# Kernel tuning notes

Measured on AMD Instinct MI355X. Metric: run time of the kernel, lower is better.

## Reference

```python
import jax, jax.numpy as jnp
from jax import lax
import numpy as np

B = 4096

def _conv(x, w, b):
    # x: [B,C,H,W], w: [O,I,3,3] torch OIHW layout, VALID, stride 1
    y = lax.conv_general_dilated(x, w, (1, 1), 'VALID',
                                 dimension_numbers=('NCHW', 'OIHW', 'NCHW'))
    return y + b[None, :, None, None]

def _pool2(x):
    return lax.reduce_window(x, -jnp.inf, lax.max, (1, 1, 2, 2), (1, 1, 2, 2), 'VALID')

def _lin(x, w, b):
    # torch Linear: y = x @ W^T + b, W: [out, in]
    return x @ w.T + b

def setup_inputs() -> dict:
    key = jax.random.key(0)
    ks = jax.random.split(key, 24)
    def w(k, shape, fan_in):
        return (jax.random.normal(k, shape, dtype=jnp.float32) / np.sqrt(fan_in)).astype(jnp.float32)
    inp = {
        'x':      jax.random.normal(ks[0], (B, 1, 28, 28), dtype=jnp.float32),
        'c1_w':   w(ks[1], (50, 1, 3, 3), 9),      'c1_b':  jnp.zeros((50,), jnp.float32),
        'c2_w':   w(ks[2], (50, 50, 3, 3), 450),   'c2_b':  jnp.zeros((50,), jnp.float32),
        'c3_w':   w(ks[3], (50, 50, 3, 3), 450),   'c3_b':  jnp.zeros((50,), jnp.float32),
        'l1c1_w': w(ks[4], (500, 50 * 13 * 13), 50 * 13 * 13), 'l1c1_b': jnp.zeros((500,), jnp.float32),
        'l2c1_w': w(ks[5], (10, 500), 500),        'l2c1_b': jnp.zeros((10,), jnp.float32),
        'l1c2_w': w(ks[6], (500, 50 * 5 * 5), 50 * 5 * 5),     'l1c2_b': jnp.zeros((500,), jnp.float32),
        'l2c2_w': w(ks[7], (10, 500), 500),        'l2c2_b': jnp.zeros((10,), jnp.float32),
        'l1_w':   w(ks[8], (500, 50), 50),         'l1_b':  jnp.zeros((500,), jnp.float32),
        'l2_w':   w(ks[9], (10, 500), 500),        'l2_b':  jnp.zeros((10,), jnp.float32),
        'd1_w':   w(ks[10], (2, 50 * 13 * 13), 50 * 13 * 13),  'd1_b':  jnp.zeros((2,), jnp.float32),
        'd2_w':   w(ks[11], (2, 50 * 5 * 5), 50 * 5 * 5),      'd2_b':  jnp.zeros((2,), jnp.float32),
    }
    return inp

def reference(x, c1_w, c1_b, c2_w, c2_b, c3_w, c3_b,
              l1c1_w, l1c1_b, l2c1_w, l2c1_b,
              l1c2_w, l1c2_b, l2c2_w, l2c2_b,
              l1_w, l1_b, l2_w, l2_b, d1_w, d1_b, d2_w, d2_b):
    b = x.shape[0]
    # stage 1
    h1 = _pool2(jax.nn.relu(_conv(x, c1_w, c1_b)))           # [B,50,13,13]
    f1 = h1.reshape(b, 50 * 13 * 13)
    exit1 = jnp.argmax(_lin(f1, d1_w, d1_b), axis=1) == 0     # [B] bool
    out1 = _lin(_lin(f1, l1c1_w, l1c1_b), l2c1_w, l2c1_b)     # [B,10] (no relu, as in source)
    # stage 2 (computed densely; selection below replicates the gather/scatter routing)
    h2 = _pool2(jax.nn.relu(_conv(h1, c2_w, c2_b)))          # [B,50,5,5]
    f2 = h2.reshape(b, 50 * 5 * 5)
    exit2 = jnp.argmax(_lin(f2, d2_w, d2_b), axis=1) == 0
    out2 = _lin(_lin(f2, l1c2_w, l1c2_b), l2c2_w, l2c2_b)
    # stage 3
    h3 = _pool2(jax.nn.relu(_conv(h2, c3_w, c3_b)))          # [B,50,1,1]
    f3 = h3.reshape(b, 50)
    out3 = _lin(jax.nn.relu(_lin(f3, l1_w, l1_b)), l2_w, l2_b)
    sel = jnp.where(exit1[:, None], out1, jnp.where(exit2[:, None], out2, out3))
    # original returns cat(out1_subset, out2_subset, out3_subset) + an index order;
    # we return the equivalent per-sample outputs in original batch order.
    return jax.nn.log_softmax(sel, axis=1)
```

## Files before the change

### kernel.cpp

```cpp
#include <hip/hip_runtime.h>
#include <hip/hip_bf16.h>
#include <cstdint>


typedef __bf16 bf16_t;
typedef __bf16 bf16x8 __attribute__((ext_vector_type(8)));
typedef float  f32x4  __attribute__((ext_vector_type(4)));

#define B_IMG 4096


__device__ void role_conv1(char* smem, int blk,
    const float* __restrict__ x, const float* __restrict__ w1,
    const float* __restrict__ b1, float* __restrict__ h1)
{
    float* ws = (float*)smem;
    float* bs = ws + 456;
    const int t = threadIdx.x;
    for (int i = t; i < 450; i += 256) ws[i] = w1[i];
    if (t < 50) bs[t] = b1[t];
    __syncthreads();

    const int idx = blk * 256 + t;
    if (idx >= B_IMG * 169) return;
    const int b   = idx / 169;
    const int pos = idx % 169;
    const int py = pos / 13, px = pos % 13;

    const float* xp = x + (size_t)b * 784 + (2 * py) * 28 + 2 * px;
    float p[4][4];
#pragma unroll
    for (int r = 0; r < 4; ++r)
#pragma unroll
        for (int c = 0; c < 4; ++c) p[r][c] = xp[r * 28 + c];

    float* hb = h1 + (size_t)b * 8480 + pos;
    if (pos < 30) h1[(size_t)b * 8480 + 8450 + pos] = 0.f;

    for (int oc = 0; oc < 50; ++oc) {
        const float* wp = &ws[oc * 9];
        const float w00 = wp[0], w01 = wp[1], w02 = wp[2];
        const float w10 = wp[3], w11 = wp[4], w12 = wp[5];
        const float w20 = wp[6], w21 = wp[7], w22 = wp[8];
        float a[2][2];
#pragma unroll
        for (int dy = 0; dy < 2; ++dy)
#pragma unroll
            for (int dx = 0; dx < 2; ++dx) {
                a[dy][dx] = p[dy + 0][dx + 0] * w00 + p[dy + 0][dx + 1] * w01 + p[dy + 0][dx + 2] * w02
                          + p[dy + 1][dx + 0] * w10 + p[dy + 1][dx + 1] * w11 + p[dy + 1][dx + 2] * w12
                          + p[dy + 2][dx + 0] * w20 + p[dy + 2][dx + 1] * w21 + p[dy + 2][dx + 2] * w22;
            }
        float v = fmaxf(fmaxf(a[0][0], a[0][1]), fmaxf(a[1][0], a[1][1])) + bs[oc];
        hb[oc * 169] = fmaxf(v, 0.f);
    }
}

__device__ void role_wb16(int blk, const float* __restrict__ src,
                          bf16_t* __restrict__ dst, int N, int K, int Kp, int total)
{
    const int idx = blk * 256 + threadIdx.x;
    if (idx >= total) return;
    const int n = idx / Kp, k = idx % Kp;
    const float v = (n < N && k < K) ? src[(size_t)n * K + k] : 0.f;
    dst[idx] = (bf16_t)v;
}

__device__ void role_w2t(int blk, const float* __restrict__ w2, float* __restrict__ w2p)
{
    const int idx = blk * 256 + threadIdx.x;
    if (idx >= 50 * 600) return;
    const int ic = idx / 600, r = idx % 600, oc = r / 12, j = r % 12;
    w2p[idx] = (j < 9) ? w2[oc * 450 + ic * 9 + j] : 0.f;
}

__device__ void role_conv2(char* smem, int b,
    const float* __restrict__ h1, const float* __restrict__ w2p,
    const float* __restrict__ b2, float* __restrict__ h2)
{
    float* in   = (float*)smem;
    float* wbuf = in + 1360;
    const int t = threadIdx.x;

    for (int s = t; s < 676; s += 256) in[s] = h1[(size_t)b * 8480 + s];
    {
        const float4* src = (const float4*)w2p;
        float4* dst = (float4*)wbuf;
        for (int s = t; s < 600; s += 256) dst[s] = src[s];
    }
    __syncthreads();
    if (t < 30) h2[(size_t)b * 1280 + 1250 + t] = 0.f;

    const int ocg = t / 25;
    const int pos = t % 25;
    const int py = pos / 5, px = pos % 5;
    const int oc0 = ocg * 5;
    const bool act = (t < 250);

    float acc[5][4];
#pragma unroll
    for (int j = 0; j < 5; ++j)
#pragma unroll
        for (int q = 0; q < 4; ++q) acc[j][q] = 0.f;

    for (int ic0 = 0; ic0 < 50; ic0 += 4) {
        const int cur = (ic0 >> 2) & 1;
        if (ic0 + 4 < 50) {
            const int nxt = cur ^ 1;
            const int nic2 = (50 - ic0 - 4 < 4) ? (50 - ic0 - 4) : 4;
            for (int s = t; s < nic2 * 169; s += 256)
                in[nxt * 680 + s] = h1[(size_t)b * 8480 + (ic0 + 4) * 169 + s];
            const float4* src = (const float4*)(w2p + (size_t)(ic0 + 4) * 600);
            float4* dst = (float4*)(wbuf + nxt * 2400);
            for (int s = t; s < nic2 * 150; s += 256) dst[s] = src[s];
        }
        if (act) {
            const int nic = (50 - ic0 < 4) ? (50 - ic0) : 4;
            const float* ibc = in + cur * 680 + (2 * py) * 13 + 2 * px;
            for (int icl = 0; icl < nic; ++icl) {
                float p[4][4];
                const float* ip = ibc + icl * 169;
#pragma unroll
                for (int r = 0; r < 4; ++r)
#pragma unroll
                    for (int c = 0; c < 4; ++c) p[r][c] = ip[r * 13 + c];
                const float* wl = wbuf + cur * 2400 + icl * 600 + oc0 * 12;
#pragma unroll
                for (int j = 0; j < 5; ++j) {
                    const f32x4 wv0 = *(const f32x4*)(wl + j * 12);
                    const f32x4 wv1 = *(const f32x4*)(wl + j * 12 + 4);
                    const f32x4 wv2 = *(const f32x4*)(wl + j * 12 + 8);
                    const float w00 = wv0[0], w01 = wv0[1], w02 = wv0[2];
                    const float w10 = wv0[3], w11 = wv1[0], w12 = wv1[1];
                    const float w20 = wv1[2], w21 = wv1[3], w22 = wv2[0];
#pragma unroll
                    for (int dy = 0; dy < 2; ++dy)
#pragma unroll
                        for (int dx = 0; dx < 2; ++dx) {
                            acc[j][dy * 2 + dx] +=
                                  p[dy + 0][dx + 0] * w00 + p[dy + 0][dx + 1] * w01 + p[dy + 0][dx + 2] * w02
                                + p[dy + 1][dx + 0] * w10 + p[dy + 1][dx + 1] * w11 + p[dy + 1][dx + 2] * w12
                                + p[dy + 2][dx + 0] * w20 + p[dy + 2][dx + 1] * w21 + p[dy + 2][dx + 2] * w22;
                        }
                }
            }
        }
        __syncthreads();
    }

    if (act) {
#pragma unroll
        for (int j = 0; j < 5; ++j) {
            float v = fmaxf(fmaxf(acc[j][0], acc[j][1]), fmaxf(acc[j][2], acc[j][3]));
            h2[(size_t)b * 1280 + (oc0 + j) * 25 + pos] = fmaxf(v + b2[oc0 + j], 0.f);
        }
    }
}

__device__ void role_conv3(char* smem, int blk,
    const float* __restrict__ h2, const float* __restrict__ w3,
    const float* __restrict__ b3, float* __restrict__ f3)
{
    float* in = (float*)smem;
    const int t = threadIdx.x;
    for (int i = t; i < 5000; i += 256) {
        const int img = i / 1250, off = i % 1250;
        in[i] = h2[(size_t)(blk * 4 + img) * 1280 + off];
    }
    __syncthreads();
    const int il = t >> 6;
    const int oc = t & 63;
    if (oc >= 50) return;

    const float* ip0 = &in[il * 1250];
    float a00 = 0.f, a01 = 0.f, a10 = 0.f, a11 = 0.f;
    for (int ic = 0; ic < 50; ++ic) {
        float p[4][4];
        const float* ip = ip0 + ic * 25;
#pragma unroll
        for (int r = 0; r < 4; ++r)
#pragma unroll
            for (int c = 0; c < 4; ++c) p[r][c] = ip[r * 5 + c];
        const float* wp = &w3[((size_t)oc * 50 + ic) * 9];
        const float w00 = wp[0], w01 = wp[1], w02 = wp[2];
        const float w10 = wp[3], w11 = wp[4], w12 = wp[5];
        const float w20 = wp[6], w21 = wp[7], w22 = wp[8];
        a00 += p[0][0]*w00 + p[0][1]*w01 + p[0][2]*w02 + p[1][0]*w10 + p[1][1]*w11 + p[1][2]*w12 + p[2][0]*w20 + p[2][1]*w21 + p[2][2]*w22;
        a01 += p[0][1]*w00 + p[0][2]*w01 + p[0][3]*w02 + p[1][1]*w10 + p[1][2]*w11 + p[1][3]*w12 + p[2][1]*w20 + p[2][2]*w21 + p[2][3]*w22;
        a10 += p[1][0]*w00 + p[1][1]*w01 + p[1][2]*w02 + p[2][0]*w10 + p[2][1]*w11 + p[2][2]*w12 + p[3][0]*w20 + p[3][1]*w21 + p[3][2]*w22;
        a11 += p[1][1]*w00 + p[1][2]*w01 + p[1][3]*w02 + p[2][1]*w10 + p[2][2]*w11 + p[2][3]*w12 + p[3][1]*w20 + p[3][2]*w21 + p[3][3]*w22;
    }
    float v = fmaxf(fmaxf(a00, a01), fmaxf(a10, a11)) + b3[oc];
    f3[(size_t)(blk * 4 + il) * 50 + oc] = fmaxf(v, 0.f);
}

__device__ void role_exit(char* smem, int b,
    const float* __restrict__ F, int ldf, int K,
    const float* __restrict__ dw, const float* __restrict__ db, int* __restrict__ e)
{
    float* r0 = (float*)smem;
    float* r1 = r0 + 256;
    const int t = threadIdx.x;
    const float* f = F + (size_t)b * ldf;
    float s0 = 0.f, s1 = 0.f;
    for (int i = t; i < K; i += 256) {
        const float v = f[i];
        s0 += v * dw[i];
        s1 += v * dw[K + i];
    }
    r0[t] = s0; r1[t] = s1;
    __syncthreads();
    for (int s = 128; s > 0; s >>= 1) {
        if (t < s) { r0[t] += r0[t + s]; r1[t] += r1[t + s]; }
        __syncthreads();
    }
    if (t == 0) e[b] = (r0[0] + db[0] >= r1[0] + db[1]) ? 1 : 0;
}

__device__ void role_gemm(char* smem, int g,
    const float* __restrict__ A, int lda, const bf16_t* __restrict__ W,
    const float* __restrict__ bias, float* __restrict__ C0, float* __restrict__ C1,
    int Kp, int khalf, int Nout, int ldc)
{
    bf16_t* As = (bf16_t*)smem;
    bf16_t* Bs = As + 128 * 40;

    const int t = threadIdx.x;
    const int m0 = (g & 31) * 128;
    const int n0 = ((g >> 5) & 7) * 64;
    const int kz = g >> 8;
    const int kbeg = kz ? khalf : 0;
    const int kend = kz ? Kp : khalf;
    float* C = kz ? C1 : C0;

    const int wave = t >> 6;
    const int lane = t & 63;
    const int wm = (wave >> 1) * 64;
    const int wn = (wave & 1) * 32;
    const int quad = lane >> 4;
    const int lr = lane & 15;

    f32x4 acc[4][2];
#pragma unroll
    for (int i = 0; i < 4; ++i)
#pragma unroll
        for (int j = 0; j < 2; ++j) acc[i][j] = (f32x4)0.f;

    const int ar = t >> 2;
    const int ac = (t & 3) * 8;

    for (int k0 = kbeg; k0 < kend; k0 += 32) {
        __syncthreads();
#pragma unroll
        for (int h = 0; h < 2; ++h) {
            const float* ap = A + (size_t)(m0 + ar + h * 64) * lda + k0 + ac;
            const float4 f0 = *(const float4*)ap;
            const float4 f1 = *(const float4*)(ap + 4);
            bf16x8 v;
            v[0] = (bf16_t)f0.x; v[1] = (bf16_t)f0.y; v[2] = (bf16_t)f0.z; v[3] = (bf16_t)f0.w;
            v[4] = (bf16_t)f1.x; v[5] = (bf16_t)f1.y; v[6] = (bf16_t)f1.z; v[7] = (bf16_t)f1.w;
            *(bf16x8*)&As[(ar + h * 64) * 40 + ac] = v;
        }
        *(uint4*)&Bs[ar * 40 + ac] = *(const uint4*)&W[(size_t)(n0 + ar) * Kp + k0 + ac];
        __syncthreads();

        bf16x8 af[4], bfr[2];
#pragma unroll
        for (int i = 0; i < 4; ++i)
            af[i] = *(const bf16x8*)&As[(wm + i * 16 + lr) * 40 + quad * 8];
#pragma unroll
        for (int j = 0; j < 2; ++j)
            bfr[j] = *(const bf16x8*)&Bs[(wn + j * 16 + lr) * 40 + quad * 8];
#pragma unroll
        for (int i = 0; i < 4; ++i)
#pragma unroll
            for (int j = 0; j < 2; ++j)
                acc[i][j] = __builtin_amdgcn_mfma_f32_16x16x32_bf16(af[i], bfr[j], acc[i][j], 0, 0, 0);
    }

#pragma unroll
    for (int j = 0; j < 2; ++j) {
        const int n = n0 + wn + j * 16 + lr;
        const float bv = (kz == 0 && n < Nout) ? bias[n] : 0.f;
#pragma unroll
        for (int i = 0; i < 4; ++i) {
            const int mrow = m0 + wm + i * 16 + quad * 4;
#pragma unroll
            for (int r = 0; r < 4; ++r)
                C[(size_t)(mrow + r) * ldc + n] = acc[i][j][r] + bv;
        }
    }
}

__device__ void role_lin10(char* smem, int blk,
    const float* __restrict__ U, const float* __restrict__ U2, int ldu,
    const float* __restrict__ W, const float* __restrict__ bias,
    float* __restrict__ out)
{
    float* red = (float*)smem;
    const int t = threadIdx.x;
    const int ks = t & 15;
    const int il = t >> 4;
    const int b  = blk * 16 + il;
    const float* u = U + (size_t)b * ldu;

    float acc[10];
#pragma unroll
    for (int o = 0; o < 10; ++o) acc[o] = 0.f;

    if (U2) {
        const float* u2 = U2 + (size_t)b * ldu;
        for (int i = 0; i < 31; ++i) {
            const int k = ks + i * 16;
            const float uv = u[k] + u2[k];
#pragma unroll
            for (int o = 0; o < 10; ++o) acc[o] += uv * W[o * 500 + k];
        }
        const int k = ks + 496;
        if (k < 500) {
            const float uv = u[k] + u2[k];
#pragma unroll
            for (int o = 0; o < 10; ++o) acc[o] += uv * W[o * 500 + k];
        }
    } else {
        for (int i = 0; i < 31; ++i) {
            const int k = ks + i * 16;
            const float uv = u[k];
#pragma unroll
            for (int o = 0; o < 10; ++o) acc[o] += uv * W[o * 500 + k];
        }
        const int k = ks + 496;
        if (k < 500) {
            const float uv = u[k];
#pragma unroll
            for (int o = 0; o < 10; ++o) acc[o] += uv * W[o * 500 + k];
        }
    }
#pragma unroll
    for (int o = 0; o < 10; ++o) red[(il * 10 + o) * 17 + ks] = acc[o];
    __syncthreads();
    if (t < 160) {
        const int il2 = t / 10, o = t - il2 * 10;
        float s = 0.f;
#pragma unroll
        for (int q = 0; q < 16; ++q) s += red[(il2 * 10 + o) * 17 + q];
        out[(size_t)(blk * 16 + il2) * 10 + o] = s + bias[o];
    }
}


__global__ __launch_bounds__(256) void k_prep(
    const float* x, const float* c1w, const float* c1b, float* h1,
    const float* l1c1w, bf16_t* Wb1, const float* l1c2w, bf16_t* Wb2,
    const float* c2w, float* w2p)
{
    extern __shared__ char smem[];
    const int g = blockIdx.x;
    if (g < 2704)        role_conv1(smem, g, x, c1w, c1b, h1);
    else if (g < 19664)  role_wb16(g - 2704, l1c1w, Wb1, 500, 8450, 8480, 512 * 8480);
    else if (g < 22224)  role_wb16(g - 19664, l1c2w, Wb2, 500, 1250, 1280, 512 * 1280);
    else                 role_w2t(g - 22224, c2w, w2p);
}

__global__ __launch_bounds__(256) void k_stage1(
    const float* h1, const bf16_t* Wb1, const float* l1c1b, float* u, float* up,
    const float* d1w, const float* d1b, int* e1,
    const float* w2p, const float* c2b, float* h2)
{
    extern __shared__ char smem[];
    const int g = blockIdx.x;
    if (g < 512)         role_gemm(smem, g, h1, 8480, Wb1, l1c1b, u, up, 8480, 4256, 500, 512);
    else if (g < 4608)   role_conv2(smem, g - 512, h1, w2p, c2b, h2);
    else                 role_exit(smem, g - 4608, h1, 8480, 8450, d1w, d1b, e1);
}

__global__ __launch_bounds__(256) void k_stage2(
    const float* h2, const bf16_t* Wb2, const float* l1c2b, float* v, float* vp,
    const float* d2w, const float* d2b, int* e2,
    const float* c3w, const float* c3b, float* f3,
    const float* u, const float* up, const float* l2c1w, const float* l2c1b, float* out1)
{
    extern __shared__ char smem[];
    const int g = blockIdx.x;
    if (g < 512)         role_gemm(smem, g, h2, 1280, Wb2, l1c2b, v, vp, 1280, 640, 500, 512);
    else if (g < 1536)   role_conv3(smem, g - 512, h2, c3w, c3b, f3);
    else if (g < 1792)   role_lin10(smem, g - 1536, u, up, 512, l2c1w, l2c1b, out1);
    else                 role_exit(smem, g - 1792, h2, 1280, 1250, d2w, d2b, e2);
}

__global__ __launch_bounds__(256) void k_tail(
    const float* __restrict__ v, const float* __restrict__ vp,
    const float* __restrict__ l2c2w, const float* __restrict__ l2c2b,
    const float* __restrict__ f3, const float* __restrict__ l1w, const float* __restrict__ l1b,
    const float* __restrict__ l2w, const float* __restrict__ l2b,
    const float* __restrict__ out1, const int* __restrict__ e1, const int* __restrict__ e2,
    float* __restrict__ out)
{
    __shared__ float fs[800];
    __shared__ float u3loc[8000];
    __shared__ float red[2720];
    __shared__ float o2loc[160];
    __shared__ float o3loc[160];

    const int t   = threadIdx.x;
    const int blk = blockIdx.x;
    const int ks  = t & 15;
    const int il  = t >> 4;

    for (int i = t; i < 800; i += 256) fs[i] = f3[(size_t)blk * 800 + i];
    __syncthreads();

    for (int im = 0; im < 16; ++im) {
        for (int o = t; o < 500; o += 256) {
            float s = 0.f;
#pragma unroll
            for (int k = 0; k < 50; ++k) s += fs[im * 50 + k] * l1w[o * 50 + k];
            u3loc[im * 500 + o] = fmaxf(s + l1b[o], 0.f);
        }
    }

    {
        const float* uu  = v  + (size_t)(blk * 16 + il) * 512;
        const float* uu2 = vp + (size_t)(blk * 16 + il) * 512;
        float acc[10];
#pragma unroll
        for (int o = 0; o < 10; ++o) acc[o] = 0.f;
        for (int i = 0; i < 31; ++i) {
            const int k = ks + i * 16;
            const float uv = uu[k] + uu2[k];
#pragma unroll
            for (int o = 0; o < 10; ++o) acc[o] += uv * l2c2w[o * 500 + k];
        }
        const int k = ks + 496;
        if (k < 500) {
            const float uv = uu[k] + uu2[k];
#pragma unroll
            for (int o = 0; o < 10; ++o) acc[o] += uv * l2c2w[o * 500 + k];
        }
        __syncthreads();
#pragma unroll
        for (int o = 0; o < 10; ++o) red[(il * 10 + o) * 17 + ks] = acc[o];
        __syncthreads();
        if (t < 160) {
            const int il2 = t / 10, o = t - il2 * 10;
            float s = 0.f;
#pragma unroll
            for (int q = 0; q < 16; ++q) s += red[(il2 * 10 + o) * 17 + q];
            o2loc[t] = s + l2c2b[o];
        }
        __syncthreads();
    }

    {
        const float* uu = u3loc + il * 500;
        float acc[10];
#pragma unroll
        for (int o = 0; o < 10; ++o) acc[o] = 0.f;
        for (int i = 0; i < 31; ++i) {
            const int k = ks + i * 16;
            const float uv = uu[k];
#pragma unroll
            for (int o = 0; o < 10; ++o) acc[o] += uv * l2w[o * 500 + k];
        }
        const int k = ks + 496;
        if (k < 500) {
            const float uv = uu[k];
#pragma unroll
            for (int o = 0; o < 10; ++o) acc[o] += uv * l2w[o * 500 + k];
        }
#pragma unroll
        for (int o = 0; o < 10; ++o) red[(il * 10 + o) * 17 + ks] = acc[o];
        __syncthreads();
        if (t < 160) {
            const int il2 = t / 10, o = t - il2 * 10;
            float s = 0.f;
#pragma unroll
            for (int q = 0; q < 16; ++q) s += red[(il2 * 10 + o) * 17 + q];
            o3loc[t] = s + l2b[o];
        }
        __syncthreads();
    }

    if (t < 16) {
        const int b = blk * 16 + t;
        float vv[10];
        if (e1[b]) {
            const float* src = out1 + (size_t)b * 10;
#pragma unroll
            for (int o = 0; o < 10; ++o) vv[o] = src[o];
        } else if (e2[b]) {
#pragma unroll
            for (int o = 0; o < 10; ++o) vv[o] = o2loc[t * 10 + o];
        } else {
#pragma unroll
            for (int o = 0; o < 10; ++o) vv[o] = o3loc[t * 10 + o];
        }
        float m = -3.4e38f;
#pragma unroll
        for (int o = 0; o < 10; ++o) m = fmaxf(m, vv[o]);
        float s = 0.f;
#pragma unroll
        for (int o = 0; o < 10; ++o) s += expf(vv[o] - m);
        const float ls = logf(s);
#pragma unroll
        for (int o = 0; o < 10; ++o) out[(size_t)b * 10 + o] = vv[o] - m - ls;
    }
}

static inline size_t align256(size_t v) { return (v + 255) & ~(size_t)255; }

extern "C" void kernel_launch(void* const* d_in, const int* in_sizes, int n_in,
                              void* d_out, int out_size, void* d_ws, size_t ws_size,
                              hipStream_t stream)
{
    const float* x     = (const float*)d_in[0];
    const float* c1w   = (const float*)d_in[1];
    const float* c1b   = (const float*)d_in[2];
    const float* c2w   = (const float*)d_in[3];
    const float* c2b   = (const float*)d_in[4];
    const float* c3w   = (const float*)d_in[5];
    const float* c3b   = (const float*)d_in[6];
    const float* l1c1w = (const float*)d_in[7];
    const float* l1c1b = (const float*)d_in[8];
    const float* l2c1w = (const float*)d_in[9];
    const float* l2c1b = (const float*)d_in[10];
    const float* l1c2w = (const float*)d_in[11];
    const float* l1c2b = (const float*)d_in[12];
    const float* l2c2w = (const float*)d_in[13];
    const float* l2c2b = (const float*)d_in[14];
    const float* l1w   = (const float*)d_in[15];
    const float* l1b   = (const float*)d_in[16];
    const float* l2w   = (const float*)d_in[17];
    const float* l2b   = (const float*)d_in[18];
    const float* d1w   = (const float*)d_in[19];
    const float* d1b   = (const float*)d_in[20];
    const float* d2w   = (const float*)d_in[21];
    const float* d2b   = (const float*)d_in[22];

    size_t off = 0;
    const size_t oWb1  = off; off = align256(off + (size_t)512 * 8480 * 2);
    const size_t oWb2  = off; off = align256(off + (size_t)512 * 1280 * 2);
    const size_t oW2P  = off; off = align256(off + (size_t)50 * 600 * 4);
    const size_t oOut1 = off; off = align256(off + (size_t)B_IMG * 10 * 4);
    const size_t oE1   = off; off = align256(off + (size_t)B_IMG * 4);
    const size_t oE2   = off; off = align256(off + (size_t)B_IMG * 4);
    const size_t oH1   = off; off = align256(off + (size_t)B_IMG * 8480 * 4);
    const size_t oH2   = off; off = align256(off + (size_t)B_IMG * 1280 * 4);
    const size_t oU    = off; off = align256(off + (size_t)B_IMG * 512 * 4);
    const size_t oUP   = off; off = align256(off + (size_t)B_IMG * 512 * 4);
    const size_t oF3   = off; off = align256(off + (size_t)B_IMG * 50 * 4);

    char* ws = (char*)d_ws;
    bf16_t* Wb1  = (bf16_t*)(ws + oWb1);
    bf16_t* Wb2  = (bf16_t*)(ws + oWb2);
    float*  w2p  = (float*) (ws + oW2P);
    float*  out1 = (float*) (ws + oOut1);
    int*    e1   = (int*)   (ws + oE1);
    int*    e2   = (int*)   (ws + oE2);
    float*  h1   = (float*) (ws + oH1);
    float*  h2   = (float*) (ws + oH2);
    float*  u    = (float*) (ws + oU);
    float*  up   = (float*) (ws + oUP);
    float*  f3   = (float*) (ws + oF3);
    float*  v    = h1;
    float*  vp   = h1 + (size_t)B_IMG * 512;

    float* out = (float*)d_out;

    k_prep<<<22342, 256, 2048, stream>>>(x, c1w, c1b, h1, l1c1w, Wb1, l1c2w, Wb2, c2w, w2p);
    k_stage1<<<8704, 256, 24832, stream>>>(h1, Wb1, l1c1b, u, up, d1w, d1b, e1, w2p, c2b, h2);
    k_stage2<<<5888, 256, 20000, stream>>>(h2, Wb2, l1c2b, v, vp, d2w, d2b, e2,
                                           c3w, c3b, f3, u, up, l2c1w, l2c1b, out1);
    k_tail<<<256, 256, 0, stream>>>(v, vp, l2c2w, l2c2b, f3, l1w, l1b, l2w, l2b,
                                    out1, e1, e2, out);

    (void)in_sizes; (void)n_in; (void)out_size; (void)ws_size;
}
```

Before: 738.5 us.

## Restructure conv2 to process two images per block with register-staged prefetch

Each conv2 block now handles two images, and each thread accumulates 10 output channels instead of 5, which halves the number of conv2 blocks and doubles per-thread reuse of the loaded input patch. Weights are no longer copied to shared memory. They are read directly from global memory (expected to hit in cache), and the input is staged in chunks of 5 channels through registers and double-buffered in shared memory. The stage-1 kernel's shared-memory request is reduced and it gets a 4-blocks-per-CU occupancy hint. The trade-offs are more register pressure from 40 accumulators plus staging registers, and weight loads that now go through the cache path instead of LDS.

```diff
diff --git a/kernel.cpp b/kernel.cpp
--- a/kernel.cpp
+++ b/kernel.cpp
@@ -74,59 +74,73 @@
     w2p[idx] = (j < 9) ? w2[oc * 450 + ic * 9 + j] : 0.f;
 }
 
-__device__ void role_conv2(char* smem, int b,
+__device__ void role_conv2(char* smem, int blkpair,
     const float* __restrict__ h1, const float* __restrict__ w2p,
     const float* __restrict__ b2, float* __restrict__ h2)
 {
-    float* in   = (float*)smem;
-    float* wbuf = in + 1360;
-    const int t = threadIdx.x;
-
-    for (int s = t; s < 676; s += 256) in[s] = h1[(size_t)b * 8480 + s];
-    {
-        const float4* src = (const float4*)w2p;
-        float4* dst = (float4*)wbuf;
-        for (int s = t; s < 600; s += 256) dst[s] = src[s];
+    float* in = (float*)smem;
+    const int t  = threadIdx.x;
+    const int b0 = blkpair * 2;
+
+    for (int s = t; s < 1690; s += 256) {
+        const int img = (s >= 845);
+        const int off = s - img * 845;
+        in[s] = h1[(size_t)(b0 + img) * 8480 + off];
     }
     __syncthreads();
-    if (t < 30) h2[(size_t)b * 1280 + 1250 + t] = 0.f;
-
-    const int ocg = t / 25;
-    const int pos = t % 25;
-    const int py = pos / 5, px = pos % 5;
-    const int oc0 = ocg * 5;
+    if (t < 60) {
+        const int img = t / 30, o = t - img * 30;
+        h2[(size_t)(b0 + img) * 1280 + 1250 + o] = 0.f;
+    }
+
+    const int il  = t / 125;
+    const int tl  = t - il * 125;
+    const int ocg = tl / 25;
+    const int pos = tl - ocg * 25;
+    const int py = pos / 5, px = pos - py * 5;
+    const int oc0 = ocg * 10;
     const bool act = (t < 250);
 
-    float acc[5][4];
-#pragma unroll
-    for (int j = 0; j < 5; ++j)
+    float acc[10][4];
+#pragma unroll
+    for (int j = 0; j < 10; ++j)
 #pragma unroll
         for (int q = 0; q < 4; ++q) acc[j][q] = 0.f;
 
-    for (int ic0 = 0; ic0 < 50; ic0 += 4) {
-        const int cur = (ic0 >> 2) & 1;
-        if (ic0 + 4 < 50) {
-            const int nxt = cur ^ 1;
-            const int nic2 = (50 - ic0 - 4 < 4) ? (50 - ic0 - 4) : 4;
-            for (int s = t; s < nic2 * 169; s += 256)
-                in[nxt * 680 + s] = h1[(size_t)b * 8480 + (ic0 + 4) * 169 + s];
-            const float4* src = (const float4*)(w2p + (size_t)(ic0 + 4) * 600);
-            float4* dst = (float4*)(wbuf + nxt * 2400);
-            for (int s = t; s < nic2 * 150; s += 256) dst[s] = src[s];
-        }
+    const float* ib0 = in + il * 845 + (2 * py) * 13 + 2 * px;
+    const float* wb0 = w2p + oc0 * 12;
+
+    for (int c = 0; c < 10; ++c) {
+        const int cur = c & 1;
+
+        float stg[7];
+        if (c + 1 < 10) {
+            const int base = (c + 1) * 845;
+#pragma unroll
+            for (int u = 0; u < 7; ++u) {
+                const int s = t + u * 256;
+                if (s < 1690) {
+                    const int img = (s >= 845);
+                    const int off = s - img * 845;
+                    stg[u] = h1[(size_t)(b0 + img) * 8480 + base + off];
+                }
+            }
+        }
+
         if (act) {
-            const int nic = (50 - ic0 < 4) ? (50 - ic0) : 4;
-            const float* ibc = in + cur * 680 + (2 * py) * 13 + 2 * px;
-            for (int icl = 0; icl < nic; ++icl) {
+            const float* ibc = ib0 + cur * 1690;
+            const int ic0 = c * 5;
+#pragma unroll 1
+            for (int icl = 0; icl < 5; ++icl) {
                 float p[4][4];
                 const float* ip = ibc + icl * 169;
 #pragma unroll
                 for (int r = 0; r < 4; ++r)
 #pragma unroll
-                    for (int c = 0; c < 4; ++c) p[r][c] = ip[r * 13 + c];
-                const float* wl = wbuf + cur * 2400 + icl * 600 + oc0 * 12;
-#pragma unroll
-                for (int j = 0; j < 5; ++j) {
+                    for (int cc = 0; cc < 4; ++cc) p[r][cc] = ip[r * 13 + cc];
+                const float* wl = wb0 + (size_t)(ic0 + icl) * 600;
+#pragma unroll
+                for (int j = 0; j < 10; ++j) {
                     const f32x4 wv0 = *(const f32x4*)(wl + j * 12);
                     const f32x4 wv1 = *(const f32x4*)(wl + j * 12 + 4);
                     const f32x4 wv2 = *(const f32x4*)(wl + j * 12 + 8);
@@ -145,14 +159,23 @@
                 }
             }
         }
+
+        if (c + 1 < 10) {
+            const int nxt = cur ^ 1;
+#pragma unroll
+            for (int u = 0; u < 7; ++u) {
+                const int s = t + u * 256;
+                if (s < 1690) in[nxt * 1690 + s] = stg[u];
+            }
+        }
         __syncthreads();
     }
 
     if (act) {
 #pragma unroll
-        for (int j = 0; j < 5; ++j) {
+        for (int j = 0; j < 10; ++j) {
             float v = fmaxf(fmaxf(acc[j][0], acc[j][1]), fmaxf(acc[j][2], acc[j][3]));
-            h2[(size_t)b * 1280 + (oc0 + j) * 25 + pos] = fmaxf(v + b2[oc0 + j], 0.f);
+            h2[(size_t)(b0 + il) * 1280 + (oc0 + j) * 25 + pos] = fmaxf(v + b2[oc0 + j], 0.f);
         }
     }
 }
@@ -362,7 +385,7 @@
     else                 role_w2t(g - 22224, c2w, w2p);
 }
 
-__global__ __launch_bounds__(256) void k_stage1(
+__global__ __launch_bounds__(256, 4) void k_stage1(
     const float* h1, const bf16_t* Wb1, const float* l1c1b, float* u, float* up,
     const float* d1w, const float* d1b, int* e1,
     const float* w2p, const float* c2b, float* h2)
@@ -370,8 +393,8 @@
     extern __shared__ char smem[];
     const int g = blockIdx.x;
     if (g < 512)         role_gemm(smem, g, h1, 8480, Wb1, l1c1b, u, up, 8480, 4256, 500, 512);
-    else if (g < 4608)   role_conv2(smem, g - 512, h1, w2p, c2b, h2);
-    else                 role_exit(smem, g - 4608, h1, 8480, 8450, d1w, d1b, e1);
+    else if (g < 2560)   role_conv2(smem, g - 512, h1, w2p, c2b, h2);
+    else                 role_exit(smem, g - 2560, h1, 8480, 8450, d1w, d1b, e1);
 }
 
 __global__ __launch_bounds__(256) void k_stage2(
@@ -568,7 +591,7 @@
     float* out = (float*)d_out;
 
     k_prep<<<22342, 256, 2048, stream>>>(x, c1w, c1b, h1, l1c1w, Wb1, l1c2w, Wb2, c2w, w2p);
-    k_stage1<<<8704, 256, 24832, stream>>>(h1, Wb1, l1c1b, u, up, d1w, d1b, e1, w2p, c2b, h2);
+    k_stage1<<<6656, 256, 15488, stream>>>(h1, Wb1, l1c1b, u, up, d1w, d1b, e1, w2p, c2b, h2);
     k_stage2<<<5888, 256, 20000, stream>>>(h2, Wb2, l1c2b, v, vp, d2w, d2b, e2,
                                            c3w, c3b, f3, u, up, l2c1w, l2c1b, out1);
     k_tail<<<256, 256, 0, stream>>>(v, vp, l2c2w, l2c2b, f3, l1w, l1b, l2w, l2b,
```

Result: slower. 982.5 us (+33.0%).

## Fuse exit-classifier dot products into conv2 and conv3 blocks

Applied to the files above, without the earlier changes.

Removes the separate exit-decision blocks by computing the exit-1 dot product inside the conv2 role, using the h1 tiles it already stages in shared memory, and the exit-2 dot product inside conv3 from its staged h2. The conv2 loop is reworked to process 5 input channels per chunk, prefetching the next chunk into registers before writing it to the other shared buffer. This drops 4096+4096 blocks and the re-reads of h1/h2 from global memory. In exchange it uses more shared memory per conv2 block and adds reduction work and register pressure to the conv blocks.

```diff
diff --git a/kernel.cpp b/kernel.cpp
--- a/kernel.cpp
+++ b/kernel.cpp
@@ -76,17 +76,20 @@
 
 __device__ void role_conv2(char* smem, int b,
     const float* __restrict__ h1, const float* __restrict__ w2p,
-    const float* __restrict__ b2, float* __restrict__ h2)
+    const float* __restrict__ b2, float* __restrict__ h2,
+    const float* __restrict__ d1w, const float* __restrict__ d1b,
+    int* __restrict__ e1)
 {
     float* in   = (float*)smem;
-    float* wbuf = in + 1360;
+    float* wbuf = in + 1696;
     const int t = threadIdx.x;
-
-    for (int s = t; s < 676; s += 256) in[s] = h1[(size_t)b * 8480 + s];
+    const float* hb = h1 + (size_t)b * 8480;
+
+    for (int s = t; s < 845; s += 256) in[s] = hb[s];
     {
         const float4* src = (const float4*)w2p;
         float4* dst = (float4*)wbuf;
-        for (int s = t; s < 600; s += 256) dst[s] = src[s];
+        for (int s = t; s < 750; s += 256) dst[s] = src[s];
     }
     __syncthreads();
     if (t < 30) h2[(size_t)b * 1280 + 1250 + t] = 0.f;
@@ -103,28 +106,42 @@
 #pragma unroll
         for (int q = 0; q < 4; ++q) acc[j][q] = 0.f;
 
-    for (int ic0 = 0; ic0 < 50; ic0 += 4) {
-        const int cur = (ic0 >> 2) & 1;
-        if (ic0 + 4 < 50) {
-            const int nxt = cur ^ 1;
-            const int nic2 = (50 - ic0 - 4 < 4) ? (50 - ic0 - 4) : 4;
-            for (int s = t; s < nic2 * 169; s += 256)
-                in[nxt * 680 + s] = h1[(size_t)b * 8480 + (ic0 + 4) * 169 + s];
-            const float4* src = (const float4*)(w2p + (size_t)(ic0 + 4) * 600);
-            float4* dst = (float4*)(wbuf + nxt * 2400);
-            for (int s = t; s < nic2 * 150; s += 256) dst[s] = src[s];
-        }
+    float ex0 = 0.f, ex1 = 0.f;
+
+    const float* ib0 = in + (2 * py) * 13 + 2 * px;
+
+    for (int c = 0; c < 10; ++c) {
+        const int cur = c & 1;
+
+        float istg[4];
+        float4 wstg[3];
+        if (c < 9) {
+            const float* isrc = hb + (c + 1) * 845;
+#pragma unroll
+            for (int u = 0; u < 4; ++u) {
+                const int s = t + u * 256;
+                if (s < 845) istg[u] = isrc[s];
+            }
+            const float4* wsrc = (const float4*)(w2p + (size_t)(c + 1) * 3000);
+#pragma unroll
+            for (int u = 0; u < 3; ++u) {
+                const int s = t + u * 256;
+                if (s < 750) wstg[u] = wsrc[s];
+            }
+        }
+
         if (act) {
-            const int nic = (50 - ic0 < 4) ? (50 - ic0) : 4;
-            const float* ibc = in + cur * 680 + (2 * py) * 13 + 2 * px;
-            for (int icl = 0; icl < nic; ++icl) {
+            const float* ibc = ib0 + cur * 845;
+            const float* wcb = wbuf + cur * 3000 + oc0 * 12;
+#pragma unroll 1
+            for (int icl = 0; icl < 5; ++icl) {
                 float p[4][4];
                 const float* ip = ibc + icl * 169;
 #pragma unroll
                 for (int r = 0; r < 4; ++r)
 #pragma unroll
-                    for (int c = 0; c < 4; ++c) p[r][c] = ip[r * 13 + c];
-                const float* wl = wbuf + cur * 2400 + icl * 600 + oc0 * 12;
+                    for (int cc = 0; cc < 4; ++cc) p[r][cc] = ip[r * 13 + cc];
+                const float* wl = wcb + icl * 600;
 #pragma unroll
                 for (int j = 0; j < 5; ++j) {
                     const f32x4 wv0 = *(const f32x4*)(wl + j * 12);
@@ -145,6 +162,36 @@
                 }
             }
         }
+
+        {
+            const float* dwa = d1w + c * 845;
+            const float* dwb = d1w + 8450 + c * 845;
+            const float* inc = in + cur * 845;
+#pragma unroll
+            for (int u = 0; u < 4; ++u) {
+                const int s = t + u * 256;
+                if (s < 845) {
+                    const float vv = inc[s];
+                    ex0 += vv * dwa[s];
+                    ex1 += vv * dwb[s];
+                }
+            }
+        }
+
+        if (c < 9) {
+            const int nxt = cur ^ 1;
+#pragma unroll
+            for (int u = 0; u < 4; ++u) {
+                const int s = t + u * 256;
+                if (s < 845) in[nxt * 845 + s] = istg[u];
+            }
+            float4* wdst = (float4*)(wbuf + nxt * 3000);
+#pragma unroll
+            for (int u = 0; u < 3; ++u) {
+                const int s = t + u * 256;
+                if (s < 750) wdst[s] = wstg[u];
+            }
+        }
         __syncthreads();
     }
 
@@ -155,11 +202,28 @@
             h2[(size_t)b * 1280 + (oc0 + j) * 25 + pos] = fmaxf(v + b2[oc0 + j], 0.f);
         }
     }
-}
-
-__device__ void role_conv3(char* smem, int blk,
+
+#pragma unroll
+    for (int off = 32; off > 0; off >>= 1) {
+        ex0 += __shfl_down(ex0, off);
+        ex1 += __shfl_down(ex1, off);
+    }
+    float* r = (float*)smem;
+    const int wv = t >> 6;
+    if ((t & 63) == 0) { r[wv] = ex0; r[8 + wv] = ex1; }
+    __syncthreads();
+    if (t == 0) {
+        const float s0 = r[0] + r[1] + r[2] + r[3] + d1b[0];
+        const float s1 = r[8] + r[9] + r[10] + r[11] + d1b[1];
+        e1[b] = (s0 >= s1) ? 1 : 0;
+    }
+}
+
+__device__ void role_conv3x(char* smem, int blk,
     const float* __restrict__ h2, const float* __restrict__ w3,
-    const float* __restrict__ b3, float* __restrict__ f3)
+    const float* __restrict__ b3,
+    const float* __restrict__ d2w, const float* __restrict__ d2b,
+    int* __restrict__ e2, float* __restrict__ f3)
 {
     float* in = (float*)smem;
     const int t = threadIdx.x;
@@ -168,8 +232,26 @@
         in[i] = h2[(size_t)(blk * 4 + img) * 1280 + off];
     }
     __syncthreads();
-    const int il = t >> 6;
-    const int oc = t & 63;
+    const int il   = t >> 6;
+    const int lane = t & 63;
+
+    {
+        const float* ip = &in[il * 1250];
+        float s0 = 0.f, s1 = 0.f;
+        for (int i = lane; i < 1250; i += 64) {
+            const float vv = ip[i];
+            s0 += vv * d2w[i];
+            s1 += vv * d2w[1250 + i];
+        }
+#pragma unroll
+        for (int off = 32; off > 0; off >>= 1) {
+            s0 += __shfl_down(s0, off);
+            s1 += __shfl_down(s1, off);
+        }
+        if (lane == 0) e2[blk * 4 + il] = (s0 + d2b[0] >= s1 + d2b[1]) ? 1 : 0;
+    }
+
+    const int oc = lane;
     if (oc >= 50) return;
 
     const float* ip0 = &in[il * 1250];
@@ -194,29 +276,6 @@
     f3[(size_t)(blk * 4 + il) * 50 + oc] = fmaxf(v, 0.f);
 }
 
-__device__ void role_exit(char* smem, int b,
-    const float* __restrict__ F, int ldf, int K,
-    const float* __restrict__ dw, const float* __restrict__ db, int* __restrict__ e)
-{
-    float* r0 = (float*)smem;
-    float* r1 = r0 + 256;
-    const int t = threadIdx.x;
-    const float* f = F + (size_t)b * ldf;
-    float s0 = 0.f, s1 = 0.f;
-    for (int i = t; i < K; i += 256) {
-        const float v = f[i];
-        s0 += v * dw[i];
-        s1 += v * dw[K + i];
-    }
-    r0[t] = s0; r1[t] = s1;
-    __syncthreads();
-    for (int s = 128; s > 0; s >>= 1) {
-        if (t < s) { r0[t] += r0[t + s]; r1[t] += r1[t + s]; }
-        __syncthreads();
-    }
-    if (t == 0) e[b] = (r0[0] + db[0] >= r1[0] + db[1]) ? 1 : 0;
-}
-
 __device__ void role_gemm(char* smem, int g,
     const float* __restrict__ A, int lda, const bf16_t* __restrict__ W,
     const float* __restrict__ bias, float* __restrict__ C0, float* __restrict__ C1,
@@ -370,8 +429,7 @@
     extern __shared__ char smem[];
     const int g = blockIdx.x;
     if (g < 512)         role_gemm(smem, g, h1, 8480, Wb1, l1c1b, u, up, 8480, 4256, 500, 512);
-    else if (g < 4608)   role_conv2(smem, g - 512, h1, w2p, c2b, h2);
-    else                 role_exit(smem, g - 4608, h1, 8480, 8450, d1w, d1b, e1);
+    else                 role_conv2(smem, g - 512, h1, w2p, c2b, h2, d1w, d1b, e1);
 }
 
 __global__ __launch_bounds__(256) void k_stage2(
@@ -383,9 +441,8 @@
     extern __shared__ char smem[];
     const int g = blockIdx.x;
     if (g < 512)         role_gemm(smem, g, h2, 1280, Wb2, l1c2b, v, vp, 1280, 640, 500, 512);
-    else if (g < 1536)   role_conv3(smem, g - 512, h2, c3w, c3b, f3);
-    else if (g < 1792)   role_lin10(smem, g - 1536, u, up, 512, l2c1w, l2c1b, out1);
-    else                 role_exit(smem, g - 1792, h2, 1280, 1250, d2w, d2b, e2);
+    else if (g < 1536)   role_conv3x(smem, g - 512, h2, c3w, c3b, d2w, d2b, e2, f3);
+    else                 role_lin10(smem, g - 1536, u, up, 512, l2c1w, l2c1b, out1);
 }
 
 __global__ __launch_bounds__(256) void k_tail(
@@ -568,8 +625,8 @@
     float* out = (float*)d_out;
 
     k_prep<<<22342, 256, 2048, stream>>>(x, c1w, c1b, h1, l1c1w, Wb1, l1c2w, Wb2, c2w, w2p);
-    k_stage1<<<8704, 256, 24832, stream>>>(h1, Wb1, l1c1b, u, up, d1w, d1b, e1, w2p, c2b, h2);
-    k_stage2<<<5888, 256, 20000, stream>>>(h2, Wb2, l1c2b, v, vp, d2w, d2b, e2,
+    k_stage1<<<4608, 256, 30784, stream>>>(h1, Wb1, l1c1b, u, up, d1w, d1b, e1, w2p, c2b, h2);
+    k_stage2<<<1792, 256, 20000, stream>>>(h2, Wb2, l1c2b, v, vp, d2w, d2b, e2,
                                            c3w, c3b, f3, u, up, l2c1w, l2c1b, out1);
     k_tail<<<256, 256, 0, stream>>>(v, vp, l2c2w, l2c2b, f3, l1w, l1b, l2w, l2b,
                                     out1, e1, e2, out);
```

Result: slower. 817.0 us (+10.6%).

## Emit bf16 activation copies for GEMMs, vectorize weight conversion, fuse exit2 into conv3

Applied to the files above, without the earlier changes.

The conv1 and conv2 producers now also write bf16 copies of their activations, so the FC GEMMs load bf16 tiles directly instead of reading fp32 and converting inside the inner loop. The weight fp32-to-bf16 prep now handles eight elements per thread with a vector store, which cuts the prep grid size. The stage-2 exit classifier is folded into the conv3 blocks using wave shuffles, since those blocks already hold the h2 tile in shared memory, and its separate blocks are removed. In exchange the producers write extra bf16 buffers, adding global write traffic and workspace.

```diff
diff --git a/kernel.cpp b/kernel.cpp
--- a/kernel.cpp
+++ b/kernel.cpp
@@ -12,7 +12,8 @@
 
 __device__ void role_conv1(char* smem, int blk,
     const float* __restrict__ x, const float* __restrict__ w1,
-    const float* __restrict__ b1, float* __restrict__ h1)
+    const float* __restrict__ b1, float* __restrict__ h1,
+    bf16_t* __restrict__ h1b)
 {
     float* ws = (float*)smem;
     float* bs = ws + 456;
@@ -34,8 +35,12 @@
 #pragma unroll
         for (int c = 0; c < 4; ++c) p[r][c] = xp[r * 28 + c];
 
-    float* hb = h1 + (size_t)b * 8480 + pos;
-    if (pos < 30) h1[(size_t)b * 8480 + 8450 + pos] = 0.f;
+    float*  hb  = h1  + (size_t)b * 8480 + pos;
+    bf16_t* hbb = h1b + (size_t)b * 8480 + pos;
+    if (pos < 30) {
+        h1 [(size_t)b * 8480 + 8450 + pos] = 0.f;
+        h1b[(size_t)b * 8480 + 8450 + pos] = (bf16_t)0.f;
+    }
 
     for (int oc = 0; oc < 50; ++oc) {
         const float* wp = &ws[oc * 9];
@@ -52,18 +57,28 @@
                           + p[dy + 2][dx + 0] * w20 + p[dy + 2][dx + 1] * w21 + p[dy + 2][dx + 2] * w22;
             }
         float v = fmaxf(fmaxf(a[0][0], a[0][1]), fmaxf(a[1][0], a[1][1])) + bs[oc];
-        hb[oc * 169] = fmaxf(v, 0.f);
-    }
-}
-
-__device__ void role_wb16(int blk, const float* __restrict__ src,
-                          bf16_t* __restrict__ dst, int N, int K, int Kp, int total)
+        const float r = fmaxf(v, 0.f);
+        hb [oc * 169] = r;
+        hbb[oc * 169] = (bf16_t)r;
+    }
+}
+
+__device__ void role_wb16v8(int blk, const float* __restrict__ src,
+                            bf16_t* __restrict__ dst, int N, int K, int Kp, int totalv)
 {
     const int idx = blk * 256 + threadIdx.x;
-    if (idx >= total) return;
-    const int n = idx / Kp, k = idx % Kp;
-    const float v = (n < N && k < K) ? src[(size_t)n * K + k] : 0.f;
-    dst[idx] = (bf16_t)v;
+    if (idx >= totalv) return;
+    const int kg = Kp >> 3;
+    const int n  = idx / kg;
+    const int k0 = (idx - n * kg) * 8;
+    bf16x8 v;
+#pragma unroll
+    for (int i = 0; i < 8; ++i) {
+        const int k = k0 + i;
+        const float f = (n < N && k < K) ? src[(size_t)n * K + k] : 0.f;
+        v[i] = (bf16_t)f;
+    }
+    *(bf16x8*)&dst[(size_t)n * Kp + k0] = v;
 }
 
 __device__ void role_w2t(int blk, const float* __restrict__ w2, float* __restrict__ w2p)
@@ -76,7 +91,8 @@
 
 __device__ void role_conv2(char* smem, int b,
     const float* __restrict__ h1, const float* __restrict__ w2p,
-    const float* __restrict__ b2, float* __restrict__ h2)
+    const float* __restrict__ b2, float* __restrict__ h2,
+    bf16_t* __restrict__ h2b)
 {
     float* in   = (float*)smem;
     float* wbuf = in + 1360;
@@ -89,7 +105,10 @@
         for (int s = t; s < 600; s += 256) dst[s] = src[s];
     }
     __syncthreads();
-    if (t < 30) h2[(size_t)b * 1280 + 1250 + t] = 0.f;
+    if (t < 30) {
+        h2 [(size_t)b * 1280 + 1250 + t] = 0.f;
+        h2b[(size_t)b * 1280 + 1250 + t] = (bf16_t)0.f;
+    }
 
     const int ocg = t / 25;
     const int pos = t % 25;
@@ -152,14 +171,18 @@
 #pragma unroll
         for (int j = 0; j < 5; ++j) {
             float v = fmaxf(fmaxf(acc[j][0], acc[j][1]), fmaxf(acc[j][2], acc[j][3]));
-            h2[(size_t)b * 1280 + (oc0 + j) * 25 + pos] = fmaxf(v + b2[oc0 + j], 0.f);
-        }
-    }
-}
-
-__device__ void role_conv3(char* smem, int blk,
+            const float r = fmaxf(v + b2[oc0 + j], 0.f);
+            h2 [(size_t)b * 1280 + (oc0 + j) * 25 + pos] = r;
+            h2b[(size_t)b * 1280 + (oc0 + j) * 25 + pos] = (bf16_t)r;
+        }
+    }
+}
+
+__device__ void role_conv3x(char* smem, int blk,
     const float* __restrict__ h2, const float* __restrict__ w3,
-    const float* __restrict__ b3, float* __restrict__ f3)
+    const float* __restrict__ b3,
+    const float* __restrict__ d2w, const float* __restrict__ d2b,
+    int* __restrict__ e2, float* __restrict__ f3)
 {
     float* in = (float*)smem;
     const int t = threadIdx.x;
@@ -168,8 +191,26 @@
         in[i] = h2[(size_t)(blk * 4 + img) * 1280 + off];
     }
     __syncthreads();
-    const int il = t >> 6;
-    const int oc = t & 63;
+    const int il   = t >> 6;
+    const int lane = t & 63;
+
+    {
+        const float* ip = &in[il * 1250];
+        float s0 = 0.f, s1 = 0.f;
+        for (int i = lane; i < 1250; i += 64) {
+            const float vv = ip[i];
+            s0 += vv * d2w[i];
+            s1 += vv * d2w[1250 + i];
+        }
+#pragma unroll
+        for (int off = 32; off > 0; off >>= 1) {
+            s0 += __shfl_down(s0, off);
+            s1 += __shfl_down(s1, off);
+        }
+        if (lane == 0) e2[blk * 4 + il] = (s0 + d2b[0] >= s1 + d2b[1]) ? 1 : 0;
+    }
+
+    const int oc = lane;
     if (oc >= 50) return;
 
     const float* ip0 = &in[il * 1250];
@@ -218,7 +259,7 @@
 }
 
 __device__ void role_gemm(char* smem, int g,
-    const float* __restrict__ A, int lda, const bf16_t* __restrict__ W,
+    const bf16_t* __restrict__ A, int lda, const bf16_t* __restrict__ W,
     const float* __restrict__ bias, float* __restrict__ C0, float* __restrict__ C1,
     int Kp, int khalf, int Nout, int ldc)
 {
@@ -253,13 +294,8 @@
         __syncthreads();
 #pragma unroll
         for (int h = 0; h < 2; ++h) {
-            const float* ap = A + (size_t)(m0 + ar + h * 64) * lda + k0 + ac;
-            const float4 f0 = *(const float4*)ap;
-            const float4 f1 = *(const float4*)(ap + 4);
-            bf16x8 v;
-            v[0] = (bf16_t)f0.x; v[1] = (bf16_t)f0.y; v[2] = (bf16_t)f0.z; v[3] = (bf16_t)f0.w;
-            v[4] = (bf16_t)f1.x; v[5] = (bf16_t)f1.y; v[6] = (bf16_t)f1.z; v[7] = (bf16_t)f1.w;
-            *(bf16x8*)&As[(ar + h * 64) * 40 + ac] = v;
+            *(uint4*)&As[(ar + h * 64) * 40 + ac] =
+                *(const uint4*)&A[(size_t)(m0 + ar + h * 64) * lda + k0 + ac];
         }
         *(uint4*)&Bs[ar * 40 + ac] = *(const uint4*)&W[(size_t)(n0 + ar) * Kp + k0 + ac];
         __syncthreads();
@@ -350,42 +386,43 @@
 
 
 __global__ __launch_bounds__(256) void k_prep(
-    const float* x, const float* c1w, const float* c1b, float* h1,
+    const float* x, const float* c1w, const float* c1b, float* h1, bf16_t* h1b,
     const float* l1c1w, bf16_t* Wb1, const float* l1c2w, bf16_t* Wb2,
     const float* c2w, float* w2p)
 {
     extern __shared__ char smem[];
     const int g = blockIdx.x;
-    if (g < 2704)        role_conv1(smem, g, x, c1w, c1b, h1);
-    else if (g < 19664)  role_wb16(g - 2704, l1c1w, Wb1, 500, 8450, 8480, 512 * 8480);
-    else if (g < 22224)  role_wb16(g - 19664, l1c2w, Wb2, 500, 1250, 1280, 512 * 1280);
-    else                 role_w2t(g - 22224, c2w, w2p);
+    if (g < 2704)        role_conv1(smem, g, x, c1w, c1b, h1, h1b);
+    else if (g < 4824)   role_wb16v8(g - 2704, l1c1w, Wb1, 500, 8450, 8480, 512 * 1060);
+    else if (g < 5144)   role_wb16v8(g - 4824, l1c2w, Wb2, 500, 1250, 1280, 512 * 160);
+    else                 role_w2t(g - 5144, c2w, w2p);
 }
 
 __global__ __launch_bounds__(256) void k_stage1(
-    const float* h1, const bf16_t* Wb1, const float* l1c1b, float* u, float* up,
+    const float* h1, const bf16_t* h1b, const bf16_t* Wb1, const float* l1c1b,
+    float* u, float* up,
     const float* d1w, const float* d1b, int* e1,
-    const float* w2p, const float* c2b, float* h2)
+    const float* w2p, const float* c2b, float* h2, bf16_t* h2b)
 {
     extern __shared__ char smem[];
     const int g = blockIdx.x;
-    if (g < 512)         role_gemm(smem, g, h1, 8480, Wb1, l1c1b, u, up, 8480, 4256, 500, 512);
-    else if (g < 4608)   role_conv2(smem, g - 512, h1, w2p, c2b, h2);
+    if (g < 512)         role_gemm(smem, g, h1b, 8480, Wb1, l1c1b, u, up, 8480, 4256, 500, 512);
+    else if (g < 4608)   role_conv2(smem, g - 512, h1, w2p, c2b, h2, h2b);
     else                 role_exit(smem, g - 4608, h1, 8480, 8450, d1w, d1b, e1);
 }
 
 __global__ __launch_bounds__(256) void k_stage2(
-    const float* h2, const bf16_t* Wb2, const float* l1c2b, float* v, float* vp,
+    const float* h2, const bf16_t* h2b, const bf16_t* Wb2, const float* l1c2b,
+    float* v, float* vp,
     const float* d2w, const float* d2b, int* e2,
     const float* c3w, const float* c3b, float* f3,
     const float* u, const float* up, const float* l2c1w, const float* l2c1b, float* out1)
 {
     extern __shared__ char smem[];
     const int g = blockIdx.x;
-    if (g < 512)         role_gemm(smem, g, h2, 1280, Wb2, l1c2b, v, vp, 1280, 640, 500, 512);
-    else if (g < 1536)   role_conv3(smem, g - 512, h2, c3w, c3b, f3);
-    else if (g < 1792)   role_lin10(smem, g - 1536, u, up, 512, l2c1w, l2c1b, out1);
-    else                 role_exit(smem, g - 1792, h2, 1280, 1250, d2w, d2b, e2);
+    if (g < 512)         role_gemm(smem, g, h2b, 1280, Wb2, l1c2b, v, vp, 1280, 640, 500, 512);
+    else if (g < 1536)   role_conv3x(smem, g - 512, h2, c3w, c3b, d2w, d2b, e2, f3);
+    else                 role_lin10(smem, g - 1536, u, up, 512, l2c1w, l2c1b, out1);
 }
 
 __global__ __launch_bounds__(256) void k_tail(
@@ -549,6 +586,8 @@
     const size_t oU    = off; off = align256(off + (size_t)B_IMG * 512 * 4);
     const size_t oUP   = off; off = align256(off + (size_t)B_IMG * 512 * 4);
     const size_t oF3   = off; off = align256(off + (size_t)B_IMG * 50 * 4);
+    const size_t oH1B  = off; off = align256(off + (size_t)B_IMG * 8480 * 2);
+    const size_t oH2B  = off; off = align256(off + (size_t)B_IMG * 1280 * 2);
 
     char* ws = (char*)d_ws;
     bf16_t* Wb1  = (bf16_t*)(ws + oWb1);
@@ -562,14 +601,18 @@
     float*  u    = (float*) (ws + oU);
     float*  up   = (float*) (ws + oUP);
     float*  f3   = (float*) (ws + oF3);
+    bf16_t* h1b  = (bf16_t*)(ws + oH1B);
+    bf16_t* h2b  = (bf16_t*)(ws + oH2B);
     float*  v    = h1;
     float*  vp   = h1 + (size_t)B_IMG * 512;
 
     float* out = (float*)d_out;
 
-    k_prep<<<22342, 256, 2048, stream>>>(x, c1w, c1b, h1, l1c1w, Wb1, l1c2w, Wb2, c2w, w2p);
-    k_stage1<<<8704, 256, 24832, stream>>>(h1, Wb1, l1c1b, u, up, d1w, d1b, e1, w2p, c2b, h2);
-    k_stage2<<<5888, 256, 20000, stream>>>(h2, Wb2, l1c2b, v, vp, d2w, d2b, e2,
+    k_prep<<<5262, 256, 2048, stream>>>(x, c1w, c1b, h1, h1b,
+                                        l1c1w, Wb1, l1c2w, Wb2, c2w, w2p);
+    k_stage1<<<8704, 256, 24832, stream>>>(h1, h1b, Wb1, l1c1b, u, up,
+                                           d1w, d1b, e1, w2p, c2b, h2, h2b);
+    k_stage2<<<1792, 256, 20000, stream>>>(h2, h2b, Wb2, l1c2b, v, vp, d2w, d2b, e2,
                                            c3w, c3b, f3, u, up, l2c1w, l2c1b, out1);
     k_tail<<<256, 256, 0, stream>>>(v, vp, l2c2w, l2c2b, f3, l1w, l1b, l2w, l2b,
                                     out1, e1, e2, out);
```

Measured after the change: 712.2 us. 1.04x faster.
